# Optimization experiments

Measured on AMD Instinct MI355X. Metric: run time of the kernel, lower is better.

Reference implementation:

```python
import jax, jax.numpy as jnp
import numpy as np

SCALE = 1.0 / (64 ** 0.5)  # 1/sqrt(dim_key)

def setup_inputs() -> dict:
    key = jax.random.key(0)
    ks = jax.random.split(key, 8)
    B, S, D, H, dk = 4, 2048, 1024, 16, 64
    s = 0.02
    return {
        "values": jax.random.normal(ks[0], (B, S, D), jnp.float32),
        "queries": jax.random.normal(ks[1], (B, S, D), jnp.float32),
        "keys": jax.random.normal(ks[2], (B, S, D), jnp.float32),
        "Wq": jax.random.normal(ks[3], (H, D, dk), jnp.float32) * s,
        "bq": jnp.zeros((H, dk), jnp.float32),
        "Wk": jax.random.normal(ks[4], (H, D, dk), jnp.float32) * s,
        "bk": jnp.zeros((H, dk), jnp.float32),
        "Wv": jax.random.normal(ks[5], (H, D, dk), jnp.float32) * s,
        "bv": jnp.zeros((H, dk), jnp.float32),
        "Wo": jax.random.normal(ks[6], (D, D), jnp.float32) * s,
        "bo": jnp.zeros((D,), jnp.float32),
    }

def reference(values, queries, keys, Wq, bq, Wk, bk, Wv, bv, Wo, bo):
    # Per-head projections, batched across heads: [B,S,D] x [H,D,dk] -> [B,H,S,dk]
    q = jnp.einsum('bsd,hdk->bhsk', queries, Wq) + bq[None, :, None, :]
    k = jnp.einsum('bsd,hdk->bhsk', keys, Wk) + bk[None, :, None, :]
    v = jnp.einsum('bsd,hdk->bhsk', values, Wv) + bv[None, :, None, :]
    # Scaled dot-product scores [B,H,S,S]
    scores = jnp.einsum('bhqk,bhsk->bhqs', q, k) * SCALE
    S = scores.shape[-1]
    causal = jnp.tril(jnp.ones((S, S), bool))
    scores = jnp.where(causal, scores, jnp.float32(-1e19))
    attn = jax.nn.softmax(scores, axis=-1)
    ctx = jnp.einsum('bhqs,bhsk->bhqk', attn, v)  # [B,H,S,dk]
    # Concat heads along last axis (head-major, matching tf.concat order)
    B, H, Sq, dk = ctx.shape
    ctx = jnp.transpose(ctx, (0, 2, 1, 3)).reshape(B, Sq, H * dk)
    return ctx @ Wo + bo
```

## Files before the change

kernel.cpp:

```cpp
#include <hip/hip_runtime.h>
#include <hip/hip_bf16.h>
#include <cstdint>

#define B_ 4
#define H_ 16
#define S_ 2048
#define D_ 1024
#define DK 64
#define QSCALE 0.18033688f

typedef float f32x4 __attribute__((ext_vector_type(4)));
typedef short bf8 __attribute__((ext_vector_type(8)));
typedef unsigned short u16;

__device__ __forceinline__ u16 f2bf(float x){
  union { float f; uint32_t u; } c; c.f = x;
  uint32_t u = c.u;
  uint32_t r = (u + 0x7FFFu + ((u >> 16) & 1u)) >> 16;
  return (u16)r;
}

__device__ __forceinline__ uint32_t pk2bf(float a, float b){
  __hip_bfloat162 t = __float22bfloat162_rn(make_float2(a, b));
  uint32_t r; __builtin_memcpy(&r, &t, 4); return r;
}

__device__ __forceinline__ void gl16(const void* g, void* l){
  __builtin_amdgcn_global_load_lds(
      (const __attribute__((address_space(1))) void*)g,
      (__attribute__((address_space(3))) void*)l, 16, 0, 0);
}

__global__ __launch_bounds__(256) void prep(
    const float* __restrict__ q, const float* __restrict__ k,
    const float* __restrict__ v, u16* __restrict__ o,
    const float* __restrict__ Wq, const float* __restrict__ Wk,
    const float* __restrict__ Wv, u16* __restrict__ oq,
    u16* __restrict__ ok, u16* __restrict__ ov,
    const float* __restrict__ Wo, u16* __restrict__ wto)
{
  __shared__ u16 T[64*72];
  const int bid = blockIdx.x;
  const int tid = threadIdx.x;
  if (bid < 3072){
    const size_t N8 = (size_t)1 << 20;
    const size_t tot = 3 * N8;
    const size_t step = (size_t)3072 * 256;
    for (size_t g0 = (size_t)bid*256 + tid; g0 < tot; g0 += step){
      int t = (int)(g0 >> 20);
      size_t r = g0 & (N8 - 1);
      const float* src = (t==0 ? q : (t==1 ? k : v));
      const float4* s4 = reinterpret_cast<const float4*>(src + r*8);
      float4 a = s4[0], b = s4[1];
      uint4 w;
      w.x = pk2bf(a.x,a.y); w.y = pk2bf(a.z,a.w);
      w.z = pk2bf(b.x,b.y); w.w = pk2bf(b.z,b.w);
      *reinterpret_cast<uint4*>(o + ((size_t)t << 23) + r*8) = w;
    }
  } else if (bid < 3072 + 768){
    const int idx = bid - 3072;
    const int z = idx >> 4, yb = idx & 15;
    const int t = z >> 4, hh = z & 15;
    const float* src = (t==0 ? Wq : t==1 ? Wk : Wv) + (size_t)hh * (D_*DK);
    u16* dst = (t==0 ? oq : t==1 ? ok : ov) + (size_t)hh * (DK*D_);
    const int r0 = yb*64;
    #pragma unroll
    for (int p=0;p<4;++p){
      int r  = p*16 + (tid>>4);
      int c4 = (tid&15)*4;
      float4 vv = *reinterpret_cast<const float4*>(&src[(size_t)(r0+r)*DK + c4]);
      uint2 w; w.x = pk2bf(vv.x, vv.y); w.y = pk2bf(vv.z, vv.w);
      *reinterpret_cast<uint2*>(&T[r*72 + c4]) = w;
    }
    __syncthreads();
    const int c = tid>>2, rg = (tid&3)*16;
    u16 tmp[16];
    #pragma unroll
    for (int i=0;i<16;++i) tmp[i] = T[(rg+i)*72 + c];
    *reinterpret_cast<bf8*>(&dst[(size_t)c*D_ + r0 + rg])     = *reinterpret_cast<bf8*>(&tmp[0]);
    *reinterpret_cast<bf8*>(&dst[(size_t)c*D_ + r0 + rg + 8]) = *reinterpret_cast<bf8*>(&tmp[8]);
  } else {
    const int idx = bid - 3840;
    const int c0 = (idx & 15)*64, r0 = (idx >> 4)*64;
    #pragma unroll
    for (int p=0;p<4;++p){
      int r  = p*16 + (tid>>4);
      int c4 = (tid&15)*4;
      float4 vv = *reinterpret_cast<const float4*>(&Wo[(size_t)(r0+r)*D_ + c0 + c4]);
      uint2 w; w.x = pk2bf(vv.x, vv.y); w.y = pk2bf(vv.z, vv.w);
      *reinterpret_cast<uint2*>(&T[r*72 + c4]) = w;
    }
    __syncthreads();
    const int c = tid>>2, rg = (tid&3)*16;
    u16 tmp[16];
    #pragma unroll
    for (int i=0;i<16;++i) tmp[i] = T[(rg+i)*72 + c];
    *reinterpret_cast<bf8*>(&wto[(size_t)(c0+c)*D_ + r0 + rg])     = *reinterpret_cast<bf8*>(&tmp[0]);
    *reinterpret_cast<bf8*>(&wto[(size_t)(c0+c)*D_ + r0 + rg + 8]) = *reinterpret_cast<bf8*>(&tmp[8]);
  }
}

__global__ __launch_bounds__(256) void gemm_qkv(
    const u16* __restrict__ Ab,
    const u16* __restrict__ Bq, const u16* __restrict__ Bk,
    const u16* __restrict__ Bv,
    const float* __restrict__ bq, const float* __restrict__ bk,
    const float* __restrict__ bv,
    u16* __restrict__ oq, u16* __restrict__ ok, u16* __restrict__ ov)
{
  __shared__ u16 As[2][128*64];
  __shared__ u16 Bs[2][128*64];
  const int tid = threadIdx.x;
  const int wid = tid>>6, lane = tid&63, g = lane>>4, l15 = lane&15;
  const int z = blockIdx.x >> 9, bid = blockIdx.x & 511;
  const u16* A     = Ab + ((size_t)z << 23);
  const u16*   Bt  = (z==0 ? Bq : z==1 ? Bk : Bv);
  const float* bias= (z==0 ? bq : z==1 ? bk : bv);
  u16* Out         = (z==0 ? oq : z==1 ? ok : ov);
  const float osc  = (z==0 ? QSCALE : 1.0f);
  const int xcd = bid & 7, i = bid >> 3;
  const int cb = i & 7, rb = xcd*8 + (i>>3);
  const int row0 = rb*128, col0 = cb*128;
  const int wr = wid>>1, wc = wid&1;

  f32x4 acc[4][4];
  #pragma unroll
  for (int m=0;m<4;++m)
    #pragma unroll
    for (int n=0;n<4;++n) acc[m][n] = (f32x4){0.f,0.f,0.f,0.f};

  auto STAGE = [&](int buf, int k0){
    #pragma unroll
    for (int p=0;p<4;++p){
      int r0l = wid*32 + p*8;
      int row = r0l + (lane>>3);
      int ch = (lane&7) ^ (row&7);
      gl16(A  + (size_t)(row0+row)*D_ + k0 + ch*8, &As[buf][r0l*64]);
      gl16(Bt + (size_t)(col0+row)*D_ + k0 + ch*8, &Bs[buf][r0l*64]);
    }
  };

  auto COMPUTE = [&](int cur){
    bf8 af[4][2], bfm[4][2];
    #pragma unroll
    for (int m=0;m<4;++m){
      int row = wr*64 + m*16 + l15;
      af[m][0] = *reinterpret_cast<const bf8*>(&As[cur][row*64 + ((g     ^(row&7))*8)]);
      af[m][1] = *reinterpret_cast<const bf8*>(&As[cur][row*64 + (((4+g) ^(row&7))*8)]);
    }
    #pragma unroll
    for (int n=0;n<4;++n){
      int row = wc*64 + n*16 + l15;
      bfm[n][0] = *reinterpret_cast<const bf8*>(&Bs[cur][row*64 + ((g     ^(row&7))*8)]);
      bfm[n][1] = *reinterpret_cast<const bf8*>(&Bs[cur][row*64 + (((4+g) ^(row&7))*8)]);
    }
    #pragma unroll
    for (int m=0;m<4;++m)
      #pragma unroll
      for (int n=0;n<4;++n){
        acc[m][n] = __builtin_amdgcn_mfma_f32_16x16x32_bf16(af[m][0], bfm[n][0], acc[m][n], 0,0,0);
        acc[m][n] = __builtin_amdgcn_mfma_f32_16x16x32_bf16(af[m][1], bfm[n][1], acc[m][n], 0,0,0);
      }
  };

  STAGE(0, 0);
  STAGE(1, 64);
  asm volatile("s_waitcnt vmcnt(8)" ::: "memory");
  asm volatile("s_barrier" ::: "memory");

  #pragma unroll 1
  for (int t = 0; t < 16; ++t){
    COMPUTE(t & 1);
    asm volatile("s_barrier" ::: "memory");
    if (t + 2 < 16){
      STAGE(t & 1, (t + 2) * 64);
      asm volatile("s_waitcnt vmcnt(8)" ::: "memory");
    } else {
      asm volatile("s_waitcnt vmcnt(0)" ::: "memory");
    }
    asm volatile("s_barrier" ::: "memory");
  }

  #pragma unroll
  for (int m=0;m<4;++m){
    #pragma unroll
    for (int n=0;n<4;++n){
      int col = col0 + wc*64 + n*16 + l15;
      float bs = bias[col];
      if (z == 2){
        int rowb = row0 + wr*64 + m*16 + g*4;
        int b = rowb>>11, s = rowb&2047;
        int h = col>>6, dkk = col&63;
        ushort4 pk;
        pk.x = f2bf(acc[m][n][0]+bs); pk.y = f2bf(acc[m][n][1]+bs);
        pk.z = f2bf(acc[m][n][2]+bs); pk.w = f2bf(acc[m][n][3]+bs);
        *reinterpret_cast<ushort4*>(&Out[(((size_t)(b*H_+h)*DK)+dkk)*S_ + s]) = pk;
      } else {
        #pragma unroll
        for (int r=0;r<4;++r){
          int row = row0 + wr*64 + m*16 + g*4 + r;
          float v = (acc[m][n][r] + bs)*osc;
          int b = row>>11, s = row&2047;
          int h = col>>6, dkk = col&63;
          Out[(((size_t)(b*H_+h)*S_)+s)*DK + dkk] = f2bf(v);
        }
      }
    }
  }
}

__global__ __launch_bounds__(256) void gemm_out(
    const u16* __restrict__ A, const u16* __restrict__ Bt,
    const float* __restrict__ bias, float* __restrict__ Outp)
{
  __shared__ u16 As[2][128*64];
  __shared__ u16 Bs[2][128*64];
  const int tid = threadIdx.x;
  const int wid = tid>>6, lane = tid&63, g = lane>>4, l15 = lane&15;
  const int bid = blockIdx.x;
  const int xcd = bid & 7, i = bid >> 3;
  const int cb = i & 7, rb = xcd*8 + (i>>3);
  const int row0 = rb*128, col0 = cb*128;
  const int wr = wid>>1, wc = wid&1;

  f32x4 acc[4][4];
  #pragma unroll
  for (int m=0;m<4;++m)
    #pragma unroll
    for (int n=0;n<4;++n) acc[m][n] = (f32x4){0.f,0.f,0.f,0.f};

  auto STAGE = [&](int buf, int k0){
    #pragma unroll
    for (int p=0;p<4;++p){
      int r0l = wid*32 + p*8;
      int row = r0l + (lane>>3);
      int ch = (lane&7) ^ (row&7);
      gl16(A  + (size_t)(row0+row)*D_ + k0 + ch*8, &As[buf][r0l*64]);
      gl16(Bt + (size_t)(col0+row)*D_ + k0 + ch*8, &Bs[buf][r0l*64]);
    }
  };

  auto COMPUTE = [&](int cur){
    bf8 af[4][2], bfm[4][2];
    #pragma unroll
    for (int m=0;m<4;++m){
      int row = wr*64 + m*16 + l15;
      af[m][0] = *reinterpret_cast<const bf8*>(&As[cur][row*64 + ((g     ^(row&7))*8)]);
      af[m][1] = *reinterpret_cast<const bf8*>(&As[cur][row*64 + (((4+g) ^(row&7))*8)]);
    }
    #pragma unroll
    for (int n=0;n<4;++n){
      int row = wc*64 + n*16 + l15;
      bfm[n][0] = *reinterpret_cast<const bf8*>(&Bs[cur][row*64 + ((g     ^(row&7))*8)]);
      bfm[n][1] = *reinterpret_cast<const bf8*>(&Bs[cur][row*64 + (((4+g) ^(row&7))*8)]);
    }
    #pragma unroll
    for (int m=0;m<4;++m)
      #pragma unroll
      for (int n=0;n<4;++n){
        acc[m][n] = __builtin_amdgcn_mfma_f32_16x16x32_bf16(af[m][0], bfm[n][0], acc[m][n], 0,0,0);
        acc[m][n] = __builtin_amdgcn_mfma_f32_16x16x32_bf16(af[m][1], bfm[n][1], acc[m][n], 0,0,0);
      }
  };

  STAGE(0, 0);
  STAGE(1, 64);
  asm volatile("s_waitcnt vmcnt(8)" ::: "memory");
  asm volatile("s_barrier" ::: "memory");

  #pragma unroll 1
  for (int t = 0; t < 16; ++t){
    COMPUTE(t & 1);
    asm volatile("s_barrier" ::: "memory");
    if (t + 2 < 16){
      STAGE(t & 1, (t + 2) * 64);
      asm volatile("s_waitcnt vmcnt(8)" ::: "memory");
    } else {
      asm volatile("s_waitcnt vmcnt(0)" ::: "memory");
    }
    asm volatile("s_barrier" ::: "memory");
  }

  #pragma unroll
  for (int m=0;m<4;++m){
    #pragma unroll
    for (int n=0;n<4;++n){
      int col = col0 + wc*64 + n*16 + l15;
      float bs = bias[col];
      #pragma unroll
      for (int r=0;r<4;++r){
        int row = row0 + wr*64 + m*16 + g*4 + r;
        Outp[(size_t)row*D_ + col] = acc[m][n][r] + bs;
      }
    }
  }
}

__global__ __launch_bounds__(256) void attn_kernel(
    const u16* __restrict__ qp, const u16* __restrict__ kp,
    const u16* __restrict__ vt, u16* __restrict__ ctx)
{
  __shared__ u16 Kl[2][64*64];
  __shared__ u16 Vl[2][64*64];
  __shared__ u16 Pl[4][32*72];
  const int tid = threadIdx.x;
  const int wid = tid>>6, lane = tid&63, g = lane>>4, l15 = lane&15;
  const int bid0 = blockIdx.x;
  const int xx = bid0 & 7, yy = bid0 >> 3;
  const int bh = xx + 8*(yy & 7);
  const int qt = 15 - (yy >> 3);
  const int b = bh >> 4, h = bh & 15;
  const size_t base = (size_t)bh * S_ * DK;

  bf8 ones;
  #pragma unroll
  for (int i=0;i<8;++i) ones[i] = (short)0x3F80;

  const int Q0 = qt*128;
  bf8 aq[2][2];
  #pragma unroll
  for (int qs=0;qs<2;++qs){
    int qrow = Q0 + wid*32 + qs*16 + l15;
    aq[qs][0] = *reinterpret_cast<const bf8*>(&qp[base + (size_t)qrow*DK +      g*8]);
    aq[qs][1] = *reinterpret_cast<const bf8*>(&qp[base + (size_t)qrow*DK + 32 + g*8]);
  }

  f32x4 acco[2][4], acc_l[2];
  #pragma unroll
  for (int qs=0;qs<2;++qs){
    #pragma unroll
    for (int nd=0;nd<4;++nd) acco[qs][nd] = (f32x4){0.f,0.f,0.f,0.f};
    acc_l[qs] = (f32x4){0.f,0.f,0.f,0.f};
  }

  auto STAGE = [&](int buf, int kt){
    const int k0 = kt*64;
    #pragma unroll
    for (int p=0;p<2;++p){
      int r0l = wid*16 + p*8;
      int row = r0l + (lane>>3);
      int ch  = (lane&7) ^ (row&7);
      gl16(kp + base + (size_t)(k0+row)*DK + ch*8, &Kl[buf][r0l*64]);
      gl16(vt + base + (size_t)row*S_ + k0 + ch*8, &Vl[buf][r0l*64]);
    }
  };

  const int nk = 2*qt + 2;
  int cur = 0;
  STAGE(cur, 0);
  asm volatile("s_waitcnt vmcnt(0)" ::: "memory");
  __syncthreads();

  for (int kt = 0; kt < nk; ++kt){
    if (kt < nk-1) STAGE(cur^1, kt+1);

    f32x4 sc[2][4];
    __builtin_amdgcn_s_setprio(1);
    #pragma unroll
    for (int n=0;n<4;++n){
      int row = n*16 + l15;
      bf8 b0 = *reinterpret_cast<const bf8*>(&Kl[cur][row*64 + ((g     ^(row&7))*8)]);
      bf8 b1 = *reinterpret_cast<const bf8*>(&Kl[cur][row*64 + (((4+g) ^(row&7))*8)]);
      #pragma unroll
      for (int qs=0;qs<2;++qs){
        f32x4 z = (f32x4){0.f,0.f,0.f,0.f};
        z = __builtin_amdgcn_mfma_f32_16x16x32_bf16(b0, aq[qs][0], z, 0,0,0);
        z = __builtin_amdgcn_mfma_f32_16x16x32_bf16(b1, aq[qs][1], z, 0,0,0);
        sc[qs][n] = z;
      }
    }
    __builtin_amdgcn_s_setprio(0);
    if (kt >= nk-2){
      const int k0 = kt*64;
      #pragma unroll
      for (int qs=0;qs<2;++qs){
        int qg = Q0 + wid*32 + qs*16 + l15;
        #pragma unroll
        for (int n=0;n<4;++n){
          #pragma unroll
          for (int r=0;r<4;++r){
            int kg = k0 + n*16 + g*4 + r;
            if (kg > qg) sc[qs][n][r] = -1e30f;
          }
        }
      }
    }
    #pragma unroll
    for (int qs=0;qs<2;++qs){
      #pragma unroll
      for (int n=0;n<4;++n){
        uint2 w;
        w.x = pk2bf(__builtin_amdgcn_exp2f(sc[qs][n][0]),
                    __builtin_amdgcn_exp2f(sc[qs][n][1]));
        w.y = pk2bf(__builtin_amdgcn_exp2f(sc[qs][n][2]),
                    __builtin_amdgcn_exp2f(sc[qs][n][3]));
        *reinterpret_cast<uint2*>(&Pl[wid][(qs*16 + l15)*72 + n*16 + g*4]) = w;
      }
    }
    asm volatile("s_waitcnt lgkmcnt(0)" ::: "memory");
    __builtin_amdgcn_sched_barrier(0);

    bf8 pa[2][2];
    __builtin_amdgcn_s_setprio(1);
    #pragma unroll
    for (int qs=0;qs<2;++qs){
      pa[qs][0] = *reinterpret_cast<const bf8*>(&Pl[wid][(qs*16 + l15)*72 +      g*8]);
      pa[qs][1] = *reinterpret_cast<const bf8*>(&Pl[wid][(qs*16 + l15)*72 + 32 + g*8]);
      acc_l[qs] = __builtin_amdgcn_mfma_f32_16x16x32_bf16(pa[qs][0], ones, acc_l[qs], 0,0,0);
      acc_l[qs] = __builtin_amdgcn_mfma_f32_16x16x32_bf16(pa[qs][1], ones, acc_l[qs], 0,0,0);
    }
    #pragma unroll
    for (int nd=0;nd<4;++nd){
      int row = nd*16 + l15;
      bf8 v0 = *reinterpret_cast<const bf8*>(&Vl[cur][row*64 + ((g     ^(row&7))*8)]);
      bf8 v1 = *reinterpret_cast<const bf8*>(&Vl[cur][row*64 + (((4+g) ^(row&7))*8)]);
      #pragma unroll
      for (int qs=0;qs<2;++qs){
        acco[qs][nd] = __builtin_amdgcn_mfma_f32_16x16x32_bf16(pa[qs][0], v0, acco[qs][nd], 0,0,0);
        acco[qs][nd] = __builtin_amdgcn_mfma_f32_16x16x32_bf16(pa[qs][1], v1, acco[qs][nd], 0,0,0);
      }
    }
    __builtin_amdgcn_s_setprio(0);
    asm volatile("s_waitcnt vmcnt(0)" ::: "memory");
    __syncthreads();
    cur ^= 1;
  }

  #pragma unroll
  for (int qs=0;qs<2;++qs){
    float rl[4];
    #pragma unroll
    for (int r=0;r<4;++r) rl[r] = __builtin_amdgcn_rcpf(acc_l[qs][r]);
    #pragma unroll
    for (int nd=0;nd<4;++nd){
      #pragma unroll
      for (int r=0;r<4;++r){
        int qg = Q0 + wid*32 + qs*16 + g*4 + r;
        float v = acco[qs][nd][r] * rl[r];
        ctx[((size_t)(b*S_) + qg)*D_ + h*DK + nd*16 + l15] = f2bf(v);
      }
    }
  }
}

extern "C" void kernel_launch(void* const* d_in, const int* in_sizes, int n_in,
                              void* d_out, int out_size, void* d_ws, size_t ws_size,
                              hipStream_t stream)
{
  const float* values  = (const float*)d_in[0];
  const float* queries = (const float*)d_in[1];
  const float* keys    = (const float*)d_in[2];
  const float* Wq = (const float*)d_in[3];
  const float* bq = (const float*)d_in[4];
  const float* Wk = (const float*)d_in[5];
  const float* bk = (const float*)d_in[6];
  const float* Wv = (const float*)d_in[7];
  const float* bv = (const float*)d_in[8];
  const float* Wo = (const float*)d_in[9];
  const float* bo = (const float*)d_in[10];
  float* out = (float*)d_out;

  const size_t NE = (size_t)B_*H_*S_*DK;
  const size_t WE = (size_t)D_*D_;
  u16* cvt = (u16*)d_ws;
  u16* qp  = cvt + 3*NE;
  u16* kp  = qp + NE;
  u16* vtb = kp + NE;
  u16* wtq = vtb + NE;
  u16* wtk = wtq + WE;
  u16* wtv = wtk + WE;
  u16* wto = wtv + WE;
  u16* ctx = cvt;

  prep<<<4096, 256, 0, stream>>>(queries, keys, values, cvt,
                                 Wq, Wk, Wv, wtq, wtk, wtv, Wo, wto);
  gemm_qkv<<<1536, 256, 0, stream>>>(cvt, wtq, wtk, wtv,
                                     bq, bk, bv, qp, kp, vtb);
  attn_kernel<<<1024, 256, 0, stream>>>(qp, kp, vtb, ctx);
  gemm_out<<<512, 256, 0, stream>>>(ctx, wto, bo, out);
}
```

Before: 171.1 us.

## Enlarge QKV GEMM tile to 256x256 with 8 waves and interleaved LDS/MFMA

The QKV projection GEMM moves from 128x128 tiles with 4 waves to 256x256 tiles with 8 waves (512 threads), using 384 blocks instead of 1536. The inner compute now loads A fragments in chunks of two and runs the MFMAs between barriers at raised wave priority, so waves stagger LDS reads and matrix math. The aim is more reuse per global and LDS load and better overlap of loads with MFMA. In exchange, LDS use doubles to 128 KB per block, which likely allows only one block per CU. The grid of 384 blocks also leaves a partial second wave across the CUs.

```diff
diff --git a/kernel.cpp b/kernel.cpp
--- a/kernel.cpp
+++ b/kernel.cpp
@@ -100,7 +100,7 @@
   }
 }
 
-__global__ __launch_bounds__(256) void gemm_qkv(
+__global__ __launch_bounds__(512, 2) void gemm_qkv(
     const u16* __restrict__ Ab,
     const u16* __restrict__ Bq, const u16* __restrict__ Bk,
     const u16* __restrict__ Bv,
@@ -108,24 +108,25 @@
     const float* __restrict__ bv,
     u16* __restrict__ oq, u16* __restrict__ ok, u16* __restrict__ ov)
 {
-  __shared__ u16 As[2][128*64];
-  __shared__ u16 Bs[2][128*64];
+  __shared__ u16 As[2][256*64];
+  __shared__ u16 Bs[2][256*64];
   const int tid = threadIdx.x;
   const int wid = tid>>6, lane = tid&63, g = lane>>4, l15 = lane&15;
-  const int z = blockIdx.x >> 9, bid = blockIdx.x & 511;
+  const int bid = blockIdx.x;
+  const int z = bid >> 7, r7 = bid & 127;
+  const int xcd = r7 & 7, i = r7 >> 3;
+  const int cb = i & 3, rb = xcd*4 + (i>>2);
   const u16* A     = Ab + ((size_t)z << 23);
   const u16*   Bt  = (z==0 ? Bq : z==1 ? Bk : Bv);
   const float* bias= (z==0 ? bq : z==1 ? bk : bv);
   u16* Out         = (z==0 ? oq : z==1 ? ok : ov);
   const float osc  = (z==0 ? QSCALE : 1.0f);
-  const int xcd = bid & 7, i = bid >> 3;
-  const int cb = i & 7, rb = xcd*8 + (i>>3);
-  const int row0 = rb*128, col0 = cb*128;
-  const int wr = wid>>1, wc = wid&1;
-
-  f32x4 acc[4][4];
-  #pragma unroll
-  for (int m=0;m<4;++m)
+  const int row0 = rb*256, col0 = cb*256;
+  const int wr = wid>>2, wc = wid&3;
+
+  f32x4 acc[8][4];
+  #pragma unroll
+  for (int m=0;m<8;++m)
     #pragma unroll
     for (int n=0;n<4;++n) acc[m][n] = (f32x4){0.f,0.f,0.f,0.f};
 
@@ -141,13 +142,7 @@
   };
 
   auto COMPUTE = [&](int cur){
-    bf8 af[4][2], bfm[4][2];
-    #pragma unroll
-    for (int m=0;m<4;++m){
-      int row = wr*64 + m*16 + l15;
-      af[m][0] = *reinterpret_cast<const bf8*>(&As[cur][row*64 + ((g     ^(row&7))*8)]);
-      af[m][1] = *reinterpret_cast<const bf8*>(&As[cur][row*64 + (((4+g) ^(row&7))*8)]);
-    }
+    bf8 bfm[4][2];
     #pragma unroll
     for (int n=0;n<4;++n){
       int row = wc*64 + n*16 + l15;
@@ -155,12 +150,29 @@
       bfm[n][1] = *reinterpret_cast<const bf8*>(&Bs[cur][row*64 + (((4+g) ^(row&7))*8)]);
     }
     #pragma unroll
-    for (int m=0;m<4;++m)
-      #pragma unroll
-      for (int n=0;n<4;++n){
-        acc[m][n] = __builtin_amdgcn_mfma_f32_16x16x32_bf16(af[m][0], bfm[n][0], acc[m][n], 0,0,0);
-        acc[m][n] = __builtin_amdgcn_mfma_f32_16x16x32_bf16(af[m][1], bfm[n][1], acc[m][n], 0,0,0);
-      }
+    for (int p=0;p<4;++p){
+      bf8 af[2][2];
+      #pragma unroll
+      for (int mm=0;mm<2;++mm){
+        int row = wr*128 + (2*p+mm)*16 + l15;
+        af[mm][0] = *reinterpret_cast<const bf8*>(&As[cur][row*64 + ((g     ^(row&7))*8)]);
+        af[mm][1] = *reinterpret_cast<const bf8*>(&As[cur][row*64 + (((4+g) ^(row&7))*8)]);
+      }
+      asm volatile("s_barrier" ::: "memory");
+      asm volatile("s_waitcnt lgkmcnt(0)" ::: "memory");
+      __builtin_amdgcn_sched_barrier(0);
+      __builtin_amdgcn_s_setprio(1);
+      #pragma unroll
+      for (int mm=0;mm<2;++mm)
+        #pragma unroll
+        for (int n=0;n<4;++n){
+          acc[2*p+mm][n] = __builtin_amdgcn_mfma_f32_16x16x32_bf16(af[mm][0], bfm[n][0], acc[2*p+mm][n], 0,0,0);
+          acc[2*p+mm][n] = __builtin_amdgcn_mfma_f32_16x16x32_bf16(af[mm][1], bfm[n][1], acc[2*p+mm][n], 0,0,0);
+        }
+      __builtin_amdgcn_s_setprio(0);
+      __builtin_amdgcn_sched_barrier(0);
+      asm volatile("s_barrier" ::: "memory");
+    }
   };
 
   STAGE(0, 0);
@@ -171,7 +183,6 @@
   #pragma unroll 1
   for (int t = 0; t < 16; ++t){
     COMPUTE(t & 1);
-    asm volatile("s_barrier" ::: "memory");
     if (t + 2 < 16){
       STAGE(t & 1, (t + 2) * 64);
       asm volatile("s_waitcnt vmcnt(8)" ::: "memory");
@@ -182,13 +193,13 @@
   }
 
   #pragma unroll
-  for (int m=0;m<4;++m){
+  for (int m=0;m<8;++m){
     #pragma unroll
     for (int n=0;n<4;++n){
       int col = col0 + wc*64 + n*16 + l15;
       float bs = bias[col];
       if (z == 2){
-        int rowb = row0 + wr*64 + m*16 + g*4;
+        int rowb = row0 + wr*128 + m*16 + g*4;
         int b = rowb>>11, s = rowb&2047;
         int h = col>>6, dkk = col&63;
         ushort4 pk;
@@ -198,7 +209,7 @@
       } else {
         #pragma unroll
         for (int r=0;r<4;++r){
-          int row = row0 + wr*64 + m*16 + g*4 + r;
+          int row = row0 + wr*128 + m*16 + g*4 + r;
           float v = (acc[m][n][r] + bs)*osc;
           int b = row>>11, s = row&2047;
           int h = col>>6, dkk = col&63;
@@ -474,8 +485,8 @@
 
   prep<<<4096, 256, 0, stream>>>(queries, keys, values, cvt,
                                  Wq, Wk, Wv, wtq, wtk, wtv, Wo, wto);
-  gemm_qkv<<<1536, 256, 0, stream>>>(cvt, wtq, wtk, wtv,
-                                     bq, bk, bv, qp, kp, vtb);
+  gemm_qkv<<<384, 512, 0, stream>>>(cvt, wtq, wtk, wtv,
+                                    bq, bk, bv, qp, kp, vtb);
   attn_kernel<<<1024, 256, 0, stream>>>(qp, kp, vtb, ctx);
   gemm_out<<<512, 256, 0, stream>>>(ctx, wto, bo, out);
 }
```

Result: slower. 189.3 us (+10.6%).
